# Performance work log

Hardware: AMD Instinct MI355X
Metric: run time of the kernel (lower is better)

## Reference

```python
import jax, jax.numpy as jnp
import numpy as np

ENT_SIZE = 100000; REL_SIZE = 500; ENT_DIM = 256; REL_DIM = 256; H = 256
E = 2048; S = 32; N = 1024; THRESHOLD = 1.0; EPS = 1e-5


def _xav(k, shape):
    fan_in = shape[-1]
    fan_out = shape[-2] if len(shape) > 1 else shape[-1]
    std = (2.0 / (fan_in + fan_out)) ** 0.5
    return jax.random.normal(k, shape, jnp.float32) * std


def setup_inputs() -> dict:
    key = jax.random.key(0)
    ks = jax.random.split(key, 16)
    inp = {}
    inp["neighbors"] = jax.random.randint(ks[0], (E, S), 0, ENT_SIZE)
    inp["pos_h"] = jax.random.randint(ks[1], (N,), 0, E)
    inp["pos_t"] = jax.random.randint(ks[2], (N,), 0, E)
    inp["pos_r"] = jax.random.randint(ks[3], (N,), 0, REL_SIZE)
    inp["neg_h"] = jax.random.randint(ks[4], (N,), 0, E)
    inp["neg_t"] = jax.random.randint(ks[5], (N,), 0, E)
    inp["neg_r"] = jax.random.randint(ks[6], (N,), 0, REL_SIZE)
    inp["ent_embed"] = _xav(ks[7], (ENT_SIZE + 1, ENT_DIM))
    inp["rel_embed"] = _xav(ks[8], (REL_SIZE, REL_DIM))
    inp["trans"] = _xav(ks[9], (2 * REL_SIZE, REL_DIM, ENT_DIM))
    inp["W_ih_f"] = _xav(ks[10], (4 * H, ENT_DIM)); inp["W_hh_f"] = _xav(ks[11], (4 * H, H))
    inp["W_ih_b"] = _xav(ks[12], (4 * H, ENT_DIM)); inp["W_hh_b"] = _xav(ks[13], (4 * H, H))
    inp["b_f"] = jnp.zeros((4 * H,), jnp.float32)
    inp["b_b"] = jnp.zeros((4 * H,), jnp.float32)
    inp["W_lin"] = _xav(ks[14], (ENT_DIM, 2 * H)); inp["b_lin"] = jnp.zeros((ENT_DIM,), jnp.float32)
    inp["gamma"] = jnp.ones((ENT_DIM,), jnp.float32); inp["beta"] = jnp.zeros((ENT_DIM,), jnp.float32)
    return inp


def _lstm_final(x, W_ih, W_hh, b):
    # x: [E,S,D] -> final hidden state [E,H] (PyTorch LSTM gate order i,f,g,o; b = b_ih+b_hh)
    h0 = jnp.zeros((x.shape[0], H), x.dtype)
    def step(carry, xt):
        h, c = carry
        g = xt @ W_ih.T + h @ W_hh.T + b  # [E,4H]
        i, f, gg, o = jnp.split(g, 4, axis=-1)
        c = jax.nn.sigmoid(f) * c + jax.nn.sigmoid(i) * jnp.tanh(gg)
        h = jax.nn.sigmoid(o) * jnp.tanh(c)
        return (h, c), None
    (h, _), _ = jax.lax.scan(step, (h0, h0), jnp.swapaxes(x, 0, 1))
    return h


def _context(ent_embed, neighbors, W_ih_f, W_hh_f, b_f, W_ih_b, W_hh_b, b_b, W_lin, b_lin, gamma, beta):
    x_seq = ent_embed[neighbors]  # [E,S,D]
    h_f = _lstm_final(x_seq, W_ih_f, W_hh_f, b_f)
    h_b = _lstm_final(x_seq[:, ::-1], W_ih_b, W_hh_b, b_b)
    lin = jnp.concatenate([h_f, h_b], -1) @ W_lin.T + b_lin  # [E,ENT_DIM]
    # BatchNorm1d in training mode: batch stats (biased variance)
    mu = lin.mean(0)
    var = lin.var(0)
    return jnp.tanh(gamma * (lin - mu) * jax.lax.rsqrt(var + EPS) + beta)


def _score(trans, rel_embed, ctx, h_idx, r_idx, t_idx):
    Wh = trans[r_idx]             # [N,REL_DIM,ENT_DIM] (grouped expert GEMV, batched)
    Wt = trans[r_idx + REL_SIZE]
    d = jnp.einsum('nre,ne->nr', Wh, ctx[h_idx]) - jnp.einsum('nre,ne->nr', Wt, ctx[t_idx])
    return jnp.linalg.norm(d + rel_embed[r_idx], axis=1)


def reference(neighbors, pos_h, pos_t, pos_r, neg_h, neg_t, neg_r,
              ent_embed, rel_embed, trans, W_ih_f, W_hh_f, W_ih_b, W_hh_b,
              b_f, b_b, W_lin, b_lin, gamma, beta):
    ctx = _context(ent_embed, neighbors, W_ih_f, W_hh_f, b_f, W_ih_b, W_hh_b, b_b,
                   W_lin, b_lin, gamma, beta)
    pos_n = _score(trans, rel_embed, ctx, pos_h, pos_r, pos_t)
    neg_n = _score(trans, rel_embed, ctx, neg_h, neg_r, neg_t)
    return jnp.sum(pos_n + jax.nn.relu(THRESHOLD - neg_n))
```

## Files before the change

### kernel.cpp

```cpp
#include <hip/hip_runtime.h>

constexpr int kE   = 2048;
constexpr int kS   = 32;
constexpr int kD   = 256;
constexpr int kG4  = 1024;
constexpr int kK   = 512;
constexpr int kREL = 500;
constexpr int kN   = 1024;

typedef unsigned short u16;
typedef __attribute__((ext_vector_type(8))) _Float16 f16x8;
typedef __attribute__((ext_vector_type(4))) float    f32x4;

static __device__ __forceinline__ u16 f2h(float f) {
  _Float16 h = (_Float16)f;
  return __builtin_bit_cast(u16, h);
}
static __device__ __forceinline__ float sigf(float x) { return 1.f / (1.f + __expf(-x)); }
static __device__ __forceinline__ float tanhfast(float x) {
  float e = __expf(2.f * x);
  return 1.f - 2.f / (e + 1.f);
}

__global__ void prep_weights(const float* __restrict__ Wih_f, const float* __restrict__ Whh_f,
                             const float* __restrict__ Wih_b, const float* __restrict__ Whh_b,
                             const float* __restrict__ Wlin_in,
                             u16* __restrict__ Wr, u16* __restrict__ Wlin) {
  int idx = blockIdx.x * 256 + threadIdx.x;
  if (idx < kG4 * kK) {
    int rp = idx >> 9, k = idx & 511;
    int g = (rp >> 4) & 3;
    int u = (rp >> 6) * 16 + (rp & 15);
    int row = g * 256 + u;
    float vf, vb;
    if (k < 256) { vf = Wih_f[row * 256 + k];        vb = Wih_b[row * 256 + k]; }
    else         { vf = Whh_f[row * 256 + k - 256];  vb = Whh_b[row * 256 + k - 256]; }
    Wr[idx] = f2h(vf);
    Wr[kG4 * kK + idx] = f2h(vb);
  }
  if (idx < 256 * kK) Wlin[idx] = f2h(Wlin_in[idx]);
}

__global__ void gather_x(const int* __restrict__ neighbors, const float* __restrict__ ent,
                         u16* __restrict__ x16) {
  const int tot = kS * kE * kD / 4;
  for (int i = blockIdx.x * blockDim.x + threadIdx.x; i < tot; i += gridDim.x * blockDim.x) {
    int k4 = i & 63;
    int row = i >> 6;
    int e = row & (kE - 1);
    int t = row >> 11;
    int nb = neighbors[e * kS + t];
    float4 v = *(const float4*)(ent + (size_t)nb * kD + k4 * 4);
    ushort4 o;
    o.x = f2h(v.x); o.y = f2h(v.y); o.z = f2h(v.z); o.w = f2h(v.w);
    *(ushort4*)(x16 + (size_t)row * kD + k4 * 4) = o;
  }
}

__global__ __launch_bounds__(256) void lstm_step_reg(
    const u16* __restrict__ x16, const u16* __restrict__ Wr,
    const float* __restrict__ b_f, const float* __restrict__ b_b,
    const u16* __restrict__ hprev, u16* __restrict__ hnext,
    float* __restrict__ cbuf, int t) {
  const int tid = threadIdx.x, lane = tid & 63, w = tid >> 6;
  const int bid = blockIdx.x;
  const int dir = bid >> 7;
  const int ut  = (bid >> 4) & 7;
  const int et  = bid & 15;
  const int wr = w >> 1, wc = w & 1;
  const int e0 = et * 128 + wr * 64;
  const int c0 = ut * 128 + wc * 64;
  const int unit = (c0 >> 6) * 16 + (lane & 15);

  const float* bd = dir ? b_b : b_f;
  const u16* Wd  = Wr + (size_t)dir * kG4 * kK;
  const u16* xs  = x16 + (size_t)(dir ? (kS - 1 - t) : t) * kE * kD;
  const u16* hpd = hprev + (size_t)dir * kE * kD;
  u16* hnd = hnext + (size_t)dir * kE * kD;
  float* cd = cbuf + (size_t)dir * kE * kD;

  const int klane = (lane >> 4) * 8;

  f32x4 acc[4][4];
#pragma unroll
  for (int m = 0; m < 4; m++)
#pragma unroll
    for (int n = 0; n < 4; n++) acc[m][n] = (f32x4){0.f, 0.f, 0.f, 0.f};

#pragma unroll
  for (int ks = 0; ks < 16; ks++) {
    const u16* asrc = (ks < 8) ? xs : hpd;
    const int ka = (ks & 7) * 32 + klane;
    f16x8 a[4], b[4];
#pragma unroll
    for (int m = 0; m < 4; m++) {
      int row = e0 + m * 16 + (lane & 15);
      a[m] = *(const f16x8*)(asrc + (size_t)row * kD + ka);
    }
#pragma unroll
    for (int n = 0; n < 4; n++) {
      int rowp = c0 + n * 16 + (lane & 15);
      b[n] = *(const f16x8*)(Wd + (size_t)rowp * kK + ks * 32 + klane);
    }
#pragma unroll
    for (int m = 0; m < 4; m++)
#pragma unroll
      for (int n = 0; n < 4; n++)
        acc[m][n] = __builtin_amdgcn_mfma_f32_16x16x32_f16(a[m], b[n], acc[m][n], 0, 0, 0);
  }

  const float bi = bd[unit], bf_ = bd[256 + unit], bg = bd[512 + unit], bo = bd[768 + unit];
#pragma unroll
  for (int m = 0; m < 4; m++)
#pragma unroll
    for (int r = 0; r < 4; r++) {
      int row = e0 + m * 16 + (lane >> 4) * 4 + r;
      size_t off = (size_t)row * kD + unit;
      float gi = acc[m][0][r] + bi;
      float gf = acc[m][1][r] + bf_;
      float gg = acc[m][2][r] + bg;
      float go = acc[m][3][r] + bo;
      float c_old = cd[off];
      float cn = sigf(gf) * c_old + sigf(gi) * tanhfast(gg);
      cd[off] = cn;
      hnd[off] = f2h(sigf(go) * tanhfast(cn));
    }
}

template <bool GMAP>
static __device__ __forceinline__ void gemm_tile(
    const u16* __restrict__ Alo, const u16* __restrict__ Ahi,
    const u16* __restrict__ W, int e0, int u0,
    u16* As, u16* Bs, f32x4 (&acc)[4][4]) {
  const int tid = threadIdx.x;
  const int lane = tid & 63;
  const int w = tid >> 6;
#pragma unroll
  for (int m = 0; m < 4; m++)
#pragma unroll
    for (int n = 0; n < 4; n++) acc[m][n] = (f32x4){0.f, 0.f, 0.f, 0.f};

  for (int ch = 0; ch < 8; ++ch) {
    const int k0 = ch * 64;
    __syncthreads();
    const u16* Asrc = (k0 < 256) ? Alo : Ahi;
    const int kbase = (k0 < 256) ? k0 : (k0 - 256);
#pragma unroll
    for (int i = 0; i < 2; i++) {
      int idx = tid + i * 256;
      int row = idx >> 3, c8 = idx & 7;
      uint4 v = *(const uint4*)(Asrc + (size_t)(e0 + row) * 256 + kbase + c8 * 8);
      *(uint4*)((char*)As + row * 128 + ((c8 * 16) ^ ((row & 7) << 4))) = v;
    }
#pragma unroll
    for (int i = 0; i < 8; i++) {
      int idx = tid + i * 256;
      int j = idx >> 3, c8 = idx & 7;
      int n = GMAP ? ((j >> 6) * 256 + u0 + (j & 63)) : j;
      uint4 v = *(const uint4*)(W + (size_t)n * kK + k0 + c8 * 8);
      *(uint4*)((char*)Bs + j * 128 + ((c8 * 16) ^ ((j & 7) << 4))) = v;
    }
    __syncthreads();
#pragma unroll
    for (int ks = 0; ks < 2; ++ks) {
      const int kb = ks * 64 + (lane >> 4) * 16;
      f16x8 a[4], b[4];
#pragma unroll
      for (int m = 0; m < 4; m++) {
        int row = m * 16 + (lane & 15);
        a[m] = *(const f16x8*)((const char*)As + row * 128 + (kb ^ ((row & 7) << 4)));
      }
#pragma unroll
      for (int n = 0; n < 4; n++) {
        int row = w * 64 + n * 16 + (lane & 15);
        b[n] = *(const f16x8*)((const char*)Bs + row * 128 + (kb ^ ((row & 7) << 4)));
      }
#pragma unroll
      for (int m = 0; m < 4; m++)
#pragma unroll
        for (int n = 0; n < 4; n++)
          acc[m][n] = __builtin_amdgcn_mfma_f32_16x16x32_f16(a[m], b[n], acc[m][n], 0, 0, 0);
    }
  }
}

__global__ __launch_bounds__(256) void lin_kernel(
    const u16* __restrict__ hf, const u16* __restrict__ hb,
    const u16* __restrict__ Wl, const float* __restrict__ b_lin,
    float* __restrict__ lin) {
  __shared__ __align__(16) char smem[40960];
  u16* As = (u16*)smem;
  u16* Bs = (u16*)(smem + 8192);
  const int tid = threadIdx.x, lane = tid & 63, w = tid >> 6;
  const int e0 = blockIdx.x * 64;
  f32x4 acc[4][4];
  gemm_tile<false>(hf, hb, Wl, e0, 0, As, Bs, acc);
#pragma unroll
  for (int m = 0; m < 4; m++)
#pragma unroll
    for (int n = 0; n < 4; n++)
#pragma unroll
      for (int r = 0; r < 4; r++) {
        int e = e0 + m * 16 + (lane >> 4) * 4 + r;
        int col = w * 64 + n * 16 + (lane & 15);
        lin[(size_t)e * 256 + col] = acc[m][n][r] + b_lin[col];
      }
}

__global__ void bn_stats(const float* __restrict__ lin, float* __restrict__ part) {
  int b = blockIdx.x, c = threadIdx.x;
  float s = 0.f, s2 = 0.f;
  for (int e = b * 256; e < b * 256 + 256; ++e) {
    float x = lin[(size_t)e * 256 + c];
    s += x; s2 += x * x;
  }
  part[b * 256 + c] = s;
  part[2048 + b * 256 + c] = s2;
}

__global__ void bn_finalize(const float* __restrict__ part, float* __restrict__ mus) {
  int c = threadIdx.x;
  float s = 0.f, s2 = 0.f;
  for (int b = 0; b < 8; b++) { s += part[b * 256 + c]; s2 += part[2048 + b * 256 + c]; }
  float mu = s * (1.f / 2048.f);
  float var = s2 * (1.f / 2048.f) - mu * mu;
  mus[c] = mu;
  mus[256 + c] = rsqrtf(var + 1e-5f);
}

__global__ void bn_tanh(const float* __restrict__ lin, const float* __restrict__ mus,
                        const float* __restrict__ gamma, const float* __restrict__ beta,
                        float* __restrict__ ctx) {
  int idx = blockIdx.x * 256 + threadIdx.x;
  int c = idx & 255;
  float x = lin[idx];
  ctx[idx] = tanhf(gamma[c] * (x - mus[c]) * mus[256 + c] + beta[c]);
}

__global__ void count_rel(const int* __restrict__ pr, const int* __restrict__ nr,
                          int* __restrict__ counts) {
  int i = blockIdx.x * 256 + threadIdx.x;
  if (i < kN) atomicAdd(&counts[pr[i]], 1);
  else if (i < 2 * kN) atomicAdd(&counts[nr[i - kN]], 1);
}

__global__ void scan_rel(const int* __restrict__ counts, int* __restrict__ offs) {
  __shared__ int s[512];
  int tid = threadIdx.x;
  s[tid] = (tid < kREL) ? counts[tid] : 0;
  __syncthreads();
  for (int d = 1; d < 512; d <<= 1) {
    int v = (tid >= d) ? s[tid - d] : 0;
    __syncthreads();
    s[tid] += v;
    __syncthreads();
  }
  if (tid == 0) offs[0] = 0;
  if (tid <= kREL) offs[tid + 1] = s[tid];
}

__global__ void scatter_rel(const int* __restrict__ pr, const int* __restrict__ nr,
                            const int* __restrict__ offs, int* __restrict__ cursor,
                            int* __restrict__ list) {
  int i = blockIdx.x * 256 + threadIdx.x;
  if (i >= 2 * kN) return;
  int r = (i < kN) ? pr[i] : nr[i - kN];
  int p = atomicAdd(&cursor[r], 1);
  list[offs[r] + p] = i;
}

__global__ __launch_bounds__(256) void score_grouped(
    const float* __restrict__ ctx, const float* __restrict__ trans,
    const float* __restrict__ rel_embed,
    const int* __restrict__ ph, const int* __restrict__ pt,
    const int* __restrict__ nh, const int* __restrict__ nt,
    const int* __restrict__ offs, const int* __restrict__ list,
    float* __restrict__ scores) {
  int r = blockIdx.x;
  int start = offs[r], end = offs[r + 1];
  if (start >= end) return;
  int tid = threadIdx.x;
  __shared__ float cs[8][2][256];
  __shared__ float red[8][4];
  float relv = rel_embed[r * 256 + tid];
  const float4* Whp = (const float4*)(trans + (size_t)r * 65536 + (size_t)tid * 256);
  const float4* Wtp = (const float4*)(trans + ((size_t)r + kREL) * 65536 + (size_t)tid * 256);

  for (int chunk = start; chunk < end; chunk += 8) {
    int G = min(8, end - chunk);
    for (int j = 0; j < G; j++) {
      int i = list[chunk + j];
      int hh = (i < kN) ? ph[i] : nh[i - kN];
      int tt = (i < kN) ? pt[i] : nt[i - kN];
      cs[j][0][tid] = ctx[(size_t)hh * 256 + tid];
      cs[j][1][tid] = ctx[(size_t)tt * 256 + tid];
    }
    __syncthreads();
    float acc[8];
#pragma unroll
    for (int j = 0; j < 8; j++) acc[j] = relv;
#pragma unroll 2
    for (int q = 0; q < 64; q++) {
      float4 w1 = Whp[q];
      float4 w2 = Wtp[q];
#pragma unroll
      for (int j = 0; j < 8; j++) {
        float4 xh = *(const float4*)&cs[j][0][q * 4];
        float4 xt = *(const float4*)&cs[j][1][q * 4];
        acc[j] += w1.x * xh.x + w1.y * xh.y + w1.z * xh.z + w1.w * xh.w
                - (w2.x * xt.x + w2.y * xt.y + w2.z * xt.z + w2.w * xt.w);
      }
    }
    for (int j = 0; j < G; j++) {
      float sq = acc[j] * acc[j];
      for (int o = 32; o; o >>= 1) sq += __shfl_down(sq, o);
      if ((tid & 63) == 0) red[j][tid >> 6] = sq;
    }
    __syncthreads();
    if (tid < G) {
      float s = red[tid][0] + red[tid][1] + red[tid][2] + red[tid][3];
      scores[list[chunk + tid]] = sqrtf(s);
    }
    __syncthreads();
  }
}

__global__ void final_reduce(const float* __restrict__ scores, float* __restrict__ out) {
  int tid = threadIdx.x;
  float a = 0.f;
  for (int i = tid; i < 2 * kN; i += 256) {
    float s = scores[i];
    a += (i < kN) ? s : fmaxf(0.f, 1.f - s);
  }
  for (int off = 32; off; off >>= 1) a += __shfl_down(a, off);
  __shared__ float w4[4];
  if ((tid & 63) == 0) w4[tid >> 6] = a;
  __syncthreads();
  if (tid == 0) out[0] = w4[0] + w4[1] + w4[2] + w4[3];
}

extern "C" void kernel_launch(void* const* d_in, const int* in_sizes, int n_in,
                              void* d_out, int out_size, void* d_ws, size_t ws_size,
                              hipStream_t stream) {
  const int*   neighbors = (const int*)d_in[0];
  const int*   pos_h = (const int*)d_in[1];
  const int*   pos_t = (const int*)d_in[2];
  const int*   pos_r = (const int*)d_in[3];
  const int*   neg_h = (const int*)d_in[4];
  const int*   neg_t = (const int*)d_in[5];
  const int*   neg_r = (const int*)d_in[6];
  const float* ent_embed = (const float*)d_in[7];
  const float* rel_embed = (const float*)d_in[8];
  const float* trans = (const float*)d_in[9];
  const float* W_ih_f = (const float*)d_in[10];
  const float* W_hh_f = (const float*)d_in[11];
  const float* W_ih_b = (const float*)d_in[12];
  const float* W_hh_b = (const float*)d_in[13];
  const float* b_f = (const float*)d_in[14];
  const float* b_b = (const float*)d_in[15];
  const float* W_lin = (const float*)d_in[16];
  const float* b_lin = (const float*)d_in[17];
  const float* gamma = (const float*)d_in[18];
  const float* beta = (const float*)d_in[19];

  char* ws = (char*)d_ws;
  size_t off = 0;
  auto alloc = [&](size_t bytes) {
    void* p = ws + off;
    off = (off + bytes + 255) & ~(size_t)255;
    return p;
  };
  u16* Wr     = (u16*)alloc((size_t)2 * kG4 * kK * 2);
  u16* Wlin   = (u16*)alloc((size_t)256 * kK * 2);
  u16* x16    = (u16*)alloc((size_t)kS * kE * kD * 2);
  u16* h0     = (u16*)alloc((size_t)2 * kE * kD * 2);
  u16* h1     = (u16*)alloc((size_t)2 * kE * kD * 2);
  float* cbuf = (float*)alloc((size_t)2 * kE * kD * 4);
  float* lin  = (float*)alloc((size_t)kE * 256 * 4);
  float* part = (float*)alloc((size_t)2 * 8 * 256 * 4);
  float* mus  = (float*)alloc((size_t)2 * 256 * 4);
  float* ctx  = (float*)alloc((size_t)kE * 256 * 4);
  float* scores = (float*)alloc((size_t)2 * kN * 4);
  int* zz     = (int*)alloc((size_t)1024 * 4);
  int* counts = zz;
  int* cursor = zz + 512;
  int* offsb  = (int*)alloc((size_t)520 * 4);
  int* list   = (int*)alloc((size_t)2 * kN * 4);
  (void)ws_size; (void)in_sizes; (void)n_in; (void)out_size;

  hipMemsetAsync(h0, 0, (size_t)2 * kE * kD * 2, stream);
  hipMemsetAsync(cbuf, 0, (size_t)2 * kE * kD * 4, stream);
  hipMemsetAsync(zz, 0, (size_t)1024 * 4, stream);

  prep_weights<<<2048, 256, 0, stream>>>(W_ih_f, W_hh_f, W_ih_b, W_hh_b, W_lin, Wr, Wlin);
  gather_x<<<4096, 256, 0, stream>>>(neighbors, ent_embed, x16);
  count_rel<<<8, 256, 0, stream>>>(pos_r, neg_r, counts);
  scan_rel<<<1, 512, 0, stream>>>(counts, offsb);
  scatter_rel<<<8, 256, 0, stream>>>(pos_r, neg_r, offsb, cursor, list);

  for (int t = 0; t < kS; ++t) {
    const u16* hp = (t & 1) ? h1 : h0;
    u16* hn = (t & 1) ? h0 : h1;
    lstm_step_reg<<<256, 256, 0, stream>>>(x16, Wr, b_f, b_b, hp, hn, cbuf, t);
  }

  lin_kernel<<<dim3(32, 1), 256, 0, stream>>>(h0, h0 + (size_t)kE * kD, Wlin, b_lin, lin);
  bn_stats<<<8, 256, 0, stream>>>(lin, part);
  bn_finalize<<<1, 256, 0, stream>>>(part, mus);
  bn_tanh<<<2048, 256, 0, stream>>>(lin, mus, gamma, beta, ctx);
  score_grouped<<<kREL, 256, 0, stream>>>(ctx, trans, rel_embed,
                                          pos_h, pos_t, neg_h, neg_t, offsb, list, scores);
  final_reduce<<<1, 256, 0, stream>>>(scores, (float*)d_out);
}
```

Baseline: 858.1 us.

## Fuse all LSTM timesteps into one persistent kernel with LDS-resident hidden state

Replaces the 32 per-timestep LSTM launches with a single kernel. Each block owns 64 entities of one direction and loops over all timesteps. The hidden state stays double-buffered in swizzled shared memory and the cell state stays in registers, which removes the global h/c round trips, per-step launches and initial memsets. Batch-norm finalize and apply are merged into one kernel, and the three relation-grouping kernels collapse into one single-block kernel. The trade-off is that only 64 blocks run, on a subset of CUs, each re-reading the full gate weights from cache every step. The 128-float accumulator per thread under a 512x2 launch bound also risks register spills.

```diff
diff --git a/kernel.cpp b/kernel.cpp
--- a/kernel.cpp
+++ b/kernel.cpp
@@ -57,80 +57,117 @@
   }
 }
 
-__global__ __launch_bounds__(256) void lstm_step_reg(
+__global__ __launch_bounds__(512, 2) void lstm_all(
     const u16* __restrict__ x16, const u16* __restrict__ Wr,
     const float* __restrict__ b_f, const float* __restrict__ b_b,
-    const u16* __restrict__ hprev, u16* __restrict__ hnext,
-    float* __restrict__ cbuf, int t) {
+    u16* __restrict__ hg) {
+  __shared__ __align__(16) char hbuf[2][32768];
   const int tid = threadIdx.x, lane = tid & 63, w = tid >> 6;
-  const int bid = blockIdx.x;
-  const int dir = bid >> 7;
-  const int ut  = (bid >> 4) & 7;
-  const int et  = bid & 15;
-  const int wr = w >> 1, wc = w & 1;
-  const int e0 = et * 128 + wr * 64;
-  const int c0 = ut * 128 + wc * 64;
-  const int unit = (c0 >> 6) * 16 + (lane & 15);
+  const int dir = blockIdx.x >> 5;
+  const int e0  = (blockIdx.x & 31) * 64;
 
   const float* bd = dir ? b_b : b_f;
-  const u16* Wd  = Wr + (size_t)dir * kG4 * kK;
-  const u16* xs  = x16 + (size_t)(dir ? (kS - 1 - t) : t) * kE * kD;
-  const u16* hpd = hprev + (size_t)dir * kE * kD;
-  u16* hnd = hnext + (size_t)dir * kE * kD;
-  float* cd = cbuf + (size_t)dir * kE * kD;
-
+  const u16* Wd = Wr + (size_t)dir * kG4 * kK;
+
+  const int u0 = w * 32 + (lane & 15);
+  float bia[2][4];
+#pragma unroll
+  for (int a = 0; a < 2; a++)
+#pragma unroll
+    for (int g = 0; g < 4; g++) bia[a][g] = bd[g * 256 + u0 + a * 16];
+
+  const int brow0 = w * 128 + (lane & 15);
   const int klane = (lane >> 4) * 8;
 
-  f32x4 acc[4][4];
+  {
+    uint4 z = {0, 0, 0, 0};
+    for (int i = tid; i < 2048; i += 512) ((uint4*)hbuf[0])[i] = z;
+  }
+  __syncthreads();
+
+  float creg[4][2][4];
 #pragma unroll
   for (int m = 0; m < 4; m++)
 #pragma unroll
-    for (int n = 0; n < 4; n++) acc[m][n] = (f32x4){0.f, 0.f, 0.f, 0.f};
-
-#pragma unroll
-  for (int ks = 0; ks < 16; ks++) {
-    const u16* asrc = (ks < 8) ? xs : hpd;
-    const int ka = (ks & 7) * 32 + klane;
-    f16x8 a[4], b[4];
-#pragma unroll
-    for (int m = 0; m < 4; m++) {
-      int row = e0 + m * 16 + (lane & 15);
-      a[m] = *(const f16x8*)(asrc + (size_t)row * kD + ka);
-    }
-#pragma unroll
-    for (int n = 0; n < 4; n++) {
-      int rowp = c0 + n * 16 + (lane & 15);
-      b[n] = *(const f16x8*)(Wd + (size_t)rowp * kK + ks * 32 + klane);
-    }
+    for (int a = 0; a < 2; a++)
+#pragma unroll
+      for (int r = 0; r < 4; r++) creg[m][a][r] = 0.f;
+
+  int cur = 0;
+  for (int t = 0; t < kS; t++) {
+    const u16* xs = x16 + (size_t)(dir ? (kS - 1 - t) : t) * kE * kD + (size_t)e0 * kD;
+    const char* hs = hbuf[cur];
+    char* hn = hbuf[cur ^ 1];
+
+    f32x4 acc[4][8];
 #pragma unroll
     for (int m = 0; m < 4; m++)
 #pragma unroll
-      for (int n = 0; n < 4; n++)
-        acc[m][n] = __builtin_amdgcn_mfma_f32_16x16x32_f16(a[m], b[n], acc[m][n], 0, 0, 0);
-  }
-
-  const float bi = bd[unit], bf_ = bd[256 + unit], bg = bd[512 + unit], bo = bd[768 + unit];
-#pragma unroll
-  for (int m = 0; m < 4; m++)
-#pragma unroll
-    for (int r = 0; r < 4; r++) {
-      int row = e0 + m * 16 + (lane >> 4) * 4 + r;
-      size_t off = (size_t)row * kD + unit;
-      float gi = acc[m][0][r] + bi;
-      float gf = acc[m][1][r] + bf_;
-      float gg = acc[m][2][r] + bg;
-      float go = acc[m][3][r] + bo;
-      float c_old = cd[off];
-      float cn = sigf(gf) * c_old + sigf(gi) * tanhfast(gg);
-      cd[off] = cn;
-      hnd[off] = f2h(sigf(go) * tanhfast(cn));
-    }
-}
-
-template <bool GMAP>
+      for (int n = 0; n < 8; n++) acc[m][n] = (f32x4){0.f, 0.f, 0.f, 0.f};
+
+#pragma unroll 4
+    for (int ks = 0; ks < 8; ks++) {
+      const int k = ks * 32 + klane;
+      f16x8 a[4], b[8];
+#pragma unroll
+      for (int m = 0; m < 4; m++)
+        a[m] = *(const f16x8*)(xs + (size_t)(m * 16 + (lane & 15)) * kD + k);
+#pragma unroll
+      for (int n = 0; n < 8; n++)
+        b[n] = *(const f16x8*)(Wd + (size_t)(brow0 + n * 16) * kK + k);
+#pragma unroll
+      for (int m = 0; m < 4; m++)
+#pragma unroll
+        for (int n = 0; n < 8; n++)
+          acc[m][n] = __builtin_amdgcn_mfma_f32_16x16x32_f16(a[m], b[n], acc[m][n], 0, 0, 0);
+    }
+#pragma unroll 4
+    for (int ks = 0; ks < 8; ks++) {
+      const int kk = ks * 32 + klane;
+      f16x8 a[4], b[8];
+#pragma unroll
+      for (int m = 0; m < 4; m++) {
+        int row = m * 16 + (lane & 15);
+        a[m] = *(const f16x8*)(hs + row * 512 + ((kk * 2) ^ ((row & 7) << 4)));
+      }
+#pragma unroll
+      for (int n = 0; n < 8; n++)
+        b[n] = *(const f16x8*)(Wd + (size_t)(brow0 + n * 16) * kK + 256 + kk);
+#pragma unroll
+      for (int m = 0; m < 4; m++)
+#pragma unroll
+        for (int n = 0; n < 8; n++)
+          acc[m][n] = __builtin_amdgcn_mfma_f32_16x16x32_f16(a[m], b[n], acc[m][n], 0, 0, 0);
+    }
+
+    const bool last = (t == kS - 1);
+#pragma unroll
+    for (int m = 0; m < 4; m++)
+#pragma unroll
+      for (int a = 0; a < 2; a++) {
+        const int unit = u0 + a * 16;
+#pragma unroll
+        for (int r = 0; r < 4; r++) {
+          float gi = acc[m][a * 4 + 0][r] + bia[a][0];
+          float gf = acc[m][a * 4 + 1][r] + bia[a][1];
+          float gg = acc[m][a * 4 + 2][r] + bia[a][2];
+          float go = acc[m][a * 4 + 3][r] + bia[a][3];
+          float cn = sigf(gf) * creg[m][a][r] + sigf(gi) * tanhfast(gg);
+          creg[m][a][r] = cn;
+          u16 hv = f2h(sigf(go) * tanhfast(cn));
+          int row = m * 16 + (lane >> 4) * 4 + r;
+          *(u16*)(hn + row * 512 + ((unit * 2) ^ ((row & 7) << 4))) = hv;
+          if (last) hg[((size_t)(dir * kE) + e0 + row) * kD + unit] = hv;
+        }
+      }
+    __syncthreads();
+    cur ^= 1;
+  }
+}
+
 static __device__ __forceinline__ void gemm_tile(
     const u16* __restrict__ Alo, const u16* __restrict__ Ahi,
-    const u16* __restrict__ W, int e0, int u0,
+    const u16* __restrict__ W, int e0,
     u16* As, u16* Bs, f32x4 (&acc)[4][4]) {
   const int tid = threadIdx.x;
   const int lane = tid & 63;
@@ -156,8 +193,7 @@
     for (int i = 0; i < 8; i++) {
       int idx = tid + i * 256;
       int j = idx >> 3, c8 = idx & 7;
-      int n = GMAP ? ((j >> 6) * 256 + u0 + (j & 63)) : j;
-      uint4 v = *(const uint4*)(W + (size_t)n * kK + k0 + c8 * 8);
+      uint4 v = *(const uint4*)(W + (size_t)j * kK + k0 + c8 * 8);
       *(uint4*)((char*)Bs + j * 128 + ((c8 * 16) ^ ((j & 7) << 4))) = v;
     }
     __syncthreads();
@@ -194,7 +230,7 @@
   const int tid = threadIdx.x, lane = tid & 63, w = tid >> 6;
   const int e0 = blockIdx.x * 64;
   f32x4 acc[4][4];
-  gemm_tile<false>(hf, hb, Wl, e0, 0, As, Bs, acc);
+  gemm_tile(hf, hb, Wl, e0, As, Bs, acc);
 #pragma unroll
   for (int m = 0; m < 4; m++)
 #pragma unroll
@@ -210,63 +246,58 @@
 __global__ void bn_stats(const float* __restrict__ lin, float* __restrict__ part) {
   int b = blockIdx.x, c = threadIdx.x;
   float s = 0.f, s2 = 0.f;
-  for (int e = b * 256; e < b * 256 + 256; ++e) {
+  for (int e = b * 32; e < b * 32 + 32; ++e) {
     float x = lin[(size_t)e * 256 + c];
     s += x; s2 += x * x;
   }
   part[b * 256 + c] = s;
-  part[2048 + b * 256 + c] = s2;
-}
-
-__global__ void bn_finalize(const float* __restrict__ part, float* __restrict__ mus) {
+  part[64 * 256 + b * 256 + c] = s2;
+}
+
+__global__ void bn_apply(const float* __restrict__ lin, const float* __restrict__ part,
+                         const float* __restrict__ gamma, const float* __restrict__ beta,
+                         float* __restrict__ ctx) {
   int c = threadIdx.x;
   float s = 0.f, s2 = 0.f;
-  for (int b = 0; b < 8; b++) { s += part[b * 256 + c]; s2 += part[2048 + b * 256 + c]; }
+  for (int b = 0; b < 64; b++) { s += part[b * 256 + c]; s2 += part[64 * 256 + b * 256 + c]; }
   float mu = s * (1.f / 2048.f);
-  float var = s2 * (1.f / 2048.f) - mu * mu;
-  mus[c] = mu;
-  mus[256 + c] = rsqrtf(var + 1e-5f);
-}
-
-__global__ void bn_tanh(const float* __restrict__ lin, const float* __restrict__ mus,
-                        const float* __restrict__ gamma, const float* __restrict__ beta,
-                        float* __restrict__ ctx) {
-  int idx = blockIdx.x * 256 + threadIdx.x;
-  int c = idx & 255;
-  float x = lin[idx];
-  ctx[idx] = tanhf(gamma[c] * (x - mus[c]) * mus[256 + c] + beta[c]);
-}
-
-__global__ void count_rel(const int* __restrict__ pr, const int* __restrict__ nr,
-                          int* __restrict__ counts) {
-  int i = blockIdx.x * 256 + threadIdx.x;
-  if (i < kN) atomicAdd(&counts[pr[i]], 1);
-  else if (i < 2 * kN) atomicAdd(&counts[nr[i - kN]], 1);
-}
-
-__global__ void scan_rel(const int* __restrict__ counts, int* __restrict__ offs) {
-  __shared__ int s[512];
+  float rsig = rsqrtf(s2 * (1.f / 2048.f) - mu * mu + 1e-5f);
+  float ga = gamma[c], be = beta[c];
+  int e0 = blockIdx.x * 8;
+  for (int e = e0; e < e0 + 8; ++e) {
+    float x = lin[(size_t)e * 256 + c];
+    ctx[(size_t)e * 256 + c] = tanhf(ga * (x - mu) * rsig + be);
+  }
+}
+
+__global__ void group_rel(const int* __restrict__ pr, const int* __restrict__ nr,
+                          int* __restrict__ offs, int* __restrict__ list) {
+  __shared__ int cnt[512], sc[512], cur[512];
   int tid = threadIdx.x;
-  s[tid] = (tid < kREL) ? counts[tid] : 0;
+  cnt[tid] = 0;
+  __syncthreads();
+  for (int i = tid; i < 2 * kN; i += 512) {
+    int r = (i < kN) ? pr[i] : nr[i - kN];
+    atomicAdd(&cnt[r], 1);
+  }
+  __syncthreads();
+  sc[tid] = cnt[tid];
   __syncthreads();
   for (int d = 1; d < 512; d <<= 1) {
-    int v = (tid >= d) ? s[tid - d] : 0;
-    __syncthreads();
-    s[tid] += v;
-    __syncthreads();
-  }
-  if (tid == 0) offs[0] = 0;
-  if (tid <= kREL) offs[tid + 1] = s[tid];
-}
-
-__global__ void scatter_rel(const int* __restrict__ pr, const int* __restrict__ nr,
-                            const int* __restrict__ offs, int* __restrict__ cursor,
-                            int* __restrict__ list) {
-  int i = blockIdx.x * 256 + threadIdx.x;
-  if (i >= 2 * kN) return;
-  int r = (i < kN) ? pr[i] : nr[i - kN];
-  int p = atomicAdd(&cursor[r], 1);
-  list[offs[r] + p] = i;
+    int v = (tid >= d) ? sc[tid - d] : 0;
+    __syncthreads();
+    sc[tid] += v;
+    __syncthreads();
+  }
+  int excl = (tid == 0) ? 0 : sc[tid - 1];
+  cur[tid] = excl;
+  if (tid <= kREL) offs[tid] = excl;
+  __syncthreads();
+  for (int i = tid; i < 2 * kN; i += 512) {
+    int r = (i < kN) ? pr[i] : nr[i - kN];
+    int p = atomicAdd(&cur[r], 1);
+    list[p] = i;
+  }
 }
 
 __global__ __launch_bounds__(256) void score_grouped(
@@ -373,41 +404,24 @@
   u16* Wr     = (u16*)alloc((size_t)2 * kG4 * kK * 2);
   u16* Wlin   = (u16*)alloc((size_t)256 * kK * 2);
   u16* x16    = (u16*)alloc((size_t)kS * kE * kD * 2);
-  u16* h0     = (u16*)alloc((size_t)2 * kE * kD * 2);
-  u16* h1     = (u16*)alloc((size_t)2 * kE * kD * 2);
-  float* cbuf = (float*)alloc((size_t)2 * kE * kD * 4);
+  u16* hg     = (u16*)alloc((size_t)2 * kE * kD * 2);
   float* lin  = (float*)alloc((size_t)kE * 256 * 4);
-  float* part = (float*)alloc((size_t)2 * 8 * 256 * 4);
-  float* mus  = (float*)alloc((size_t)2 * 256 * 4);
+  float* part = (float*)alloc((size_t)2 * 64 * 256 * 4);
   float* ctx  = (float*)alloc((size_t)kE * 256 * 4);
   float* scores = (float*)alloc((size_t)2 * kN * 4);
-  int* zz     = (int*)alloc((size_t)1024 * 4);
-  int* counts = zz;
-  int* cursor = zz + 512;
-  int* offsb  = (int*)alloc((size_t)520 * 4);
+  int* offsb  = (int*)alloc((size_t)512 * 4);
   int* list   = (int*)alloc((size_t)2 * kN * 4);
   (void)ws_size; (void)in_sizes; (void)n_in; (void)out_size;
 
-  hipMemsetAsync(h0, 0, (size_t)2 * kE * kD * 2, stream);
-  hipMemsetAsync(cbuf, 0, (size_t)2 * kE * kD * 4, stream);
-  hipMemsetAsync(zz, 0, (size_t)1024 * 4, stream);
-
   prep_weights<<<2048, 256, 0, stream>>>(W_ih_f, W_hh_f, W_ih_b, W_hh_b, W_lin, Wr, Wlin);
   gather_x<<<4096, 256, 0, stream>>>(neighbors, ent_embed, x16);
-  count_rel<<<8, 256, 0, stream>>>(pos_r, neg_r, counts);
-  scan_rel<<<1, 512, 0, stream>>>(counts, offsb);
-  scatter_rel<<<8, 256, 0, stream>>>(pos_r, neg_r, offsb, cursor, list);
-
-  for (int t = 0; t < kS; ++t) {
-    const u16* hp = (t & 1) ? h1 : h0;
-    u16* hn = (t & 1) ? h0 : h1;
-    lstm_step_reg<<<256, 256, 0, stream>>>(x16, Wr, b_f, b_b, hp, hn, cbuf, t);
-  }
-
-  lin_kernel<<<dim3(32, 1), 256, 0, stream>>>(h0, h0 + (size_t)kE * kD, Wlin, b_lin, lin);
-  bn_stats<<<8, 256, 0, stream>>>(lin, part);
-  bn_finalize<<<1, 256, 0, stream>>>(part, mus);
-  bn_tanh<<<2048, 256, 0, stream>>>(lin, mus, gamma, beta, ctx);
+  group_rel<<<1, 512, 0, stream>>>(pos_r, neg_r, offsb, list);
+
+  lstm_all<<<64, 512, 0, stream>>>(x16, Wr, b_f, b_b, hg);
+
+  lin_kernel<<<32, 256, 0, stream>>>(hg, hg + (size_t)kE * kD, Wlin, b_lin, lin);
+  bn_stats<<<64, 256, 0, stream>>>(lin, part);
+  bn_apply<<<256, 256, 0, stream>>>(lin, part, gamma, beta, ctx);
   score_grouped<<<kREL, 256, 0, stream>>>(ctx, trans, rel_embed,
                                           pos_h, pos_t, neg_h, neg_t, offsb, list, scores);
   final_reduce<<<1, 256, 0, stream>>>(scores, (float*)d_out);
```

New measurement: 1.977 ms. 2.3x slower.
